# Kernel tuning notes

Measured on AMD Instinct MI355X. Metric: run time of the kernel, lower is better.

Reference implementation:

```python
import math
import jax
import jax.numpy as jnp
import numpy as np

B, L, C = 16, 512, 1024
N_HEAD = 8
HEAD = C // N_HEAD


def setup_inputs() -> dict:
    key = jax.random.key(0)
    k1, k2, k3, k4, k5, k6 = jax.random.split(key, 6)
    x = jax.random.normal(k1, (B, L, C), dtype=jnp.float32)
    # binary adjacency (0/1) as float, as in graph data
    adj = jax.random.randint(k2, (B, L, L), 0, 2).astype(jnp.float32)
    W_qkv = jax.random.normal(k3, (C, 3 * C), dtype=jnp.float32) * (1.0 / math.sqrt(C))
    b_qkv = jax.random.normal(k4, (3 * C,), dtype=jnp.float32) * 0.02
    W_d = jax.random.normal(k5, (1, C), dtype=jnp.float32)
    b_d = jax.random.normal(k6, (C,), dtype=jnp.float32) * 0.02
    return {"x": x, "adj": adj, "W_qkv": W_qkv, "b_qkv": b_qkv, "W_d": W_d, "b_d": b_d}


def reference(x, adj, W_qkv, b_qkv, W_d, b_d):
    # degree gating (self.degree == True)
    degree = adj.sum(-1, keepdims=True)                      # [B,L,1]
    gate = jax.nn.sigmoid(degree @ W_d + b_d)                # [B,L,C]
    x = x * gate
    # fused qkv projection, chunk into qk / res / value
    qkv = x @ W_qkv + b_qkv                                  # [B,L,3C]
    qk, res, value = jnp.split(qkv, 3, axis=-1)
    def heads(t):                                            # [B,L,C] -> [B,H,L,hd]
        return t.reshape(B, L, N_HEAD, HEAD).transpose(0, 2, 1, 3)
    qk, res, value = heads(qk), heads(res), heads(value)
    qk = jax.nn.sigmoid(qk)
    # sigmoid-kernel attention scores
    attn = jnp.einsum("bhld,bhmd->bhlm", qk, qk) / math.sqrt(HEAD)
    # adjacency masking (rel_pos_bias == True)
    attn = jnp.where(adj[:, None, :, :] == 0, 0.0, attn)
    # sum-normalization instead of softmax
    attn = attn / (attn.sum(-1, keepdims=True) + 1e-6)
    out = jnp.einsum("bhlm,bhmd->bhld", attn, value) + res   # residual from qkv chunk
    out = out.transpose(0, 2, 1, 3).reshape(B, L, C)
    return jax.nn.relu(out)
```

## Files before the change

kernel.cpp:

```cpp
#include <hip/hip_runtime.h>
#include <math.h>

#define BDIM 16
#define LDIM 512
#define CDIM 1024
#define NH 8
#define HD 128
#define MROWS (BDIM * LDIM)
#define N3 (3 * CDIM)

typedef unsigned short u16;
typedef unsigned long long u64;
typedef short s8v __attribute__((ext_vector_type(8)));
typedef short s4v __attribute__((ext_vector_type(4)));
typedef float f32x4 __attribute__((ext_vector_type(4)));

__device__ __forceinline__ float sigmoidf_(float z) {
    return 1.0f / (1.0f + __expf(-z));
}
__device__ __forceinline__ u16 f2bf(float f) {
    union { float f; unsigned int u; } v; v.f = f;
    unsigned int u = v.u;
    unsigned int r = (u + 0x7FFFu + ((u >> 16) & 1u)) >> 16;
    return (u16)r;
}
__device__ __forceinline__ float bf2f(u16 b) {
    union { unsigned int u; float f; } v; v.u = ((unsigned int)b) << 16;
    return v.f;
}

__global__ __launch_bounds__(256) void pre_kernel(const float* __restrict__ adj,
                                                  const float* __restrict__ x,
                                                  const float* __restrict__ Wd,
                                                  const float* __restrict__ bd,
                                                  const float* __restrict__ W,
                                                  u16* __restrict__ xg,
                                                  u64* __restrict__ adjbits,
                                                  u16* __restrict__ Wt) {
    __shared__ float wsum[4];
    __shared__ float tile[64][65];
    int t = threadIdx.x;
    if (blockIdx.x < MROWS) {
        int row = blockIdx.x;
        int w = t >> 6, lane = t & 63;
        const float* a = adj + (size_t)row * LDIM;
        float v0 = a[w * 128 + lane];
        float v1 = a[w * 128 + 64 + lane];
        u64 b0 = __ballot(v0 != 0.f);
        u64 b1 = __ballot(v1 != 0.f);
        if (lane == 0) {
            adjbits[(size_t)row * (LDIM / 64) + 2 * w]     = b0;
            adjbits[(size_t)row * (LDIM / 64) + 2 * w + 1] = b1;
        }
        float s = v0 + v1;
        #pragma unroll
        for (int off = 32; off > 0; off >>= 1) s += __shfl_down(s, off);
        if (lane == 0) wsum[w] = s;
        __syncthreads();
        float d = wsum[0] + wsum[1] + wsum[2] + wsum[3];

        float4 xv = ((const float4*)(x + (size_t)row * CDIM))[t];
        float4 wv = ((const float4*)Wd)[t];
        float4 bv = ((const float4*)bd)[t];
        s4v o;
        o.x = (short)f2bf(xv.x * sigmoidf_(d * wv.x + bv.x));
        o.y = (short)f2bf(xv.y * sigmoidf_(d * wv.y + bv.y));
        o.z = (short)f2bf(xv.z * sigmoidf_(d * wv.z + bv.z));
        o.w = (short)f2bf(xv.w * sigmoidf_(d * wv.w + bv.w));
        ((s4v*)(xg + (size_t)row * CDIM))[t] = o;
    } else {
        int bid = blockIdx.x - MROWS;
        int k0 = (bid & 15) * 64, n0 = (bid >> 4) * 64;
        int tx = t & 63, ty = t >> 6;
        #pragma unroll
        for (int yy = ty; yy < 64; yy += 4)
            tile[yy][tx] = W[(size_t)(k0 + yy) * N3 + n0 + tx];
        __syncthreads();
        #pragma unroll
        for (int yy = ty; yy < 64; yy += 4)
            Wt[(size_t)(n0 + yy) * CDIM + k0 + tx] = f2bf(tile[tx][yy]);
    }
}

__global__ __launch_bounds__(256, 3) void gemm_bf16_kernel(const u16* __restrict__ A,
                                                           const u16* __restrict__ Bt,
                                                           const float* __restrict__ bias,
                                                           u16* __restrict__ ksig,
                                                           u16* __restrict__ resb,
                                                           u16* __restrict__ vt) {
    __shared__ __align__(16) u16 As[128 * 64];
    __shared__ __align__(16) u16 Bs[128 * 64];
    int t = threadIdx.x;
    int m0 = blockIdx.y * 128, n0 = blockIdx.x * 128;
    int lane = t & 63, w = t >> 6;
    int i15 = lane & 15, quad = lane >> 4;
    int wm = w >> 1, wn = w & 1;

    f32x4 acc[4][4];
    #pragma unroll
    for (int i = 0; i < 4; ++i)
        #pragma unroll
        for (int j = 0; j < 4; ++j) acc[i][j] = (f32x4)(0.f);

    for (int k0 = 0; k0 < CDIM; k0 += 64) {
        #pragma unroll
        for (int p = 0; p < 4; ++p) {
            int sb = (w * 4 + p) * 64;
            int s = sb + lane;
            int row = s >> 3;
            int seg = (s & 7) ^ (row & 7);
            const u16* ga = A + (size_t)(m0 + row) * CDIM + k0 + seg * 8;
            const u16* gb = Bt + (size_t)(n0 + row) * CDIM + k0 + seg * 8;
            __builtin_amdgcn_global_load_lds(
                (const __attribute__((address_space(1))) unsigned int*)ga,
                (__attribute__((address_space(3))) unsigned int*)&As[sb * 8], 16, 0, 0);
            __builtin_amdgcn_global_load_lds(
                (const __attribute__((address_space(1))) unsigned int*)gb,
                (__attribute__((address_space(3))) unsigned int*)&Bs[sb * 8], 16, 0, 0);
        }
        __syncthreads();
        #pragma unroll
        for (int kc = 0; kc < 2; ++kc) {
            s8v aF[4], bF[4];
            #pragma unroll
            for (int mt = 0; mt < 4; ++mt) {
                int row = wm * 64 + mt * 16 + i15;
                int slot = row * 8 + ((kc * 4 + quad) ^ (i15 & 7));
                aF[mt] = *(const s8v*)&As[slot * 8];
            }
            #pragma unroll
            for (int nt = 0; nt < 4; ++nt) {
                int row = wn * 64 + nt * 16 + i15;
                int slot = row * 8 + ((kc * 4 + quad) ^ (i15 & 7));
                bF[nt] = *(const s8v*)&Bs[slot * 8];
            }
            #pragma unroll
            for (int mt = 0; mt < 4; ++mt)
                #pragma unroll
                for (int nt = 0; nt < 4; ++nt)
                    acc[mt][nt] = __builtin_amdgcn_mfma_f32_16x16x32_bf16(aF[mt], bF[nt], acc[mt][nt], 0, 0, 0);
        }
        __syncthreads();
    }

    int chunk = n0 >> 10;
    #pragma unroll
    for (int nt = 0; nt < 4; ++nt) {
        int ncol = n0 + wn * 64 + nt * 16 + i15;
        float bv = bias[ncol];
        #pragma unroll
        for (int mt = 0; mt < 4; ++mt) {
            int mbase = m0 + wm * 64 + mt * 16 + quad * 4;
            if (chunk == 0) {
                int h = (ncol >> 7) & 7, d = ncol & 127;
                #pragma unroll
                for (int r = 0; r < 4; ++r) {
                    int mrow = mbase + r;
                    int bb = mrow >> 9, l = mrow & 511;
                    ksig[(((size_t)bb * NH + h) * LDIM + l) * HD + d] = f2bf(sigmoidf_(acc[mt][nt][r] + bv));
                }
            } else if (chunk == 1) {
                #pragma unroll
                for (int r = 0; r < 4; ++r) {
                    int mrow = mbase + r;
                    resb[(size_t)mrow * CDIM + (ncol - CDIM)] = f2bf(acc[mt][nt][r] + bv);
                }
            } else {
                int h = (ncol >> 7) & 7, d = ncol & 127;
                int bb = mbase >> 9, l = mbase & 511;
                s4v pk;
                pk.x = (short)f2bf(acc[mt][nt][0] + bv);
                pk.y = (short)f2bf(acc[mt][nt][1] + bv);
                pk.z = (short)f2bf(acc[mt][nt][2] + bv);
                pk.w = (short)f2bf(acc[mt][nt][3] + bv);
                *(s4v*)&vt[(((size_t)bb * NH + h) * HD + d) * LDIM + l] = pk;
            }
        }
    }
}

#define MT 32
#define NITER (LDIM / MT)
__global__ __launch_bounds__(256) void attn_kernel(const u16* __restrict__ ksig,
                                                   const u16* __restrict__ vt,
                                                   const u16* __restrict__ resb,
                                                   const u64* __restrict__ adjbits,
                                                   float* __restrict__ out) {
    __shared__ __align__(16) u16 lds_ks[2][MT * 128];
    __shared__ __align__(16) u16 lds_vt[2][128 * MT];
    __shared__ __align__(16) u16 lds_ps[4][16][40];

    int t = threadIdx.x;
    int lane = t & 63, w = t >> 6;
    int i15 = lane & 15, quad = lane >> 4;
    int bid = blockIdx.x;
    int l0 = (bid >> 7) * 64;
    int b  = (bid >> 3) & 15;
    int h  = bid & 7;

    const u16* ksig_bh = ksig + ((size_t)b * NH + h) * LDIM * HD;
    const u16* vt_bh   = vt + ((size_t)b * NH + h) * HD * LDIM;
    const unsigned int* abits32 = (const unsigned int*)adjbits;
    size_t arow0 = ((size_t)b * LDIM + l0 + w * 16 + quad * 4) * (LDIM / 32);

    s8v aQ[4];
    {
        const u16* qrow = ksig_bh + (size_t)(l0 + w * 16 + i15) * HD + quad * 8;
        #pragma unroll
        for (int kc = 0; kc < 4; ++kc) aQ[kc] = *(const s8v*)(qrow + kc * 32);
    }

    f32x4 accO[8];
    #pragma unroll
    for (int i = 0; i < 8; ++i) accO[i] = (f32x4)(0.f);
    float prs[4] = {0.f, 0.f, 0.f, 0.f};

    const float scale = 0.08838834764831845f;

    auto stage = [&](int m0s, int buf) {
        #pragma unroll
        for (int p = 0; p < 2; ++p) {
            int sb = (w * 2 + p) * 64;
            int s = sb + lane;
            int row = s >> 4;
            int seg = (s & 15) ^ (row & 15);
            const u16* g = ksig_bh + (size_t)(m0s + row) * HD + seg * 8;
            __builtin_amdgcn_global_load_lds(
                (const __attribute__((address_space(1))) unsigned int*)g,
                (__attribute__((address_space(3))) unsigned int*)&lds_ks[buf][sb * 8], 16, 0, 0);
        }
        #pragma unroll
        for (int p = 0; p < 2; ++p) {
            int sb = (w * 2 + p) * 64;
            int s = sb + lane;
            int row = s >> 2;
            int seg = (s & 3) ^ ((row >> 1) & 3);
            const u16* g = vt_bh + (size_t)row * LDIM + m0s + seg * 8;
            __builtin_amdgcn_global_load_lds(
                (const __attribute__((address_space(1))) unsigned int*)g,
                (__attribute__((address_space(3))) unsigned int*)&lds_vt[buf][sb * 8], 16, 0, 0);
        }
    };

    stage(0, 0);
    __syncthreads();

    for (int i = 0; i < NITER; ++i) {
        int cur = i & 1;
        int m0 = i * MT;
        if (i + 1 < NITER) stage(m0 + MT, cur ^ 1);

        unsigned int mw[4];
        #pragma unroll
        for (int r = 0; r < 4; ++r)
            mw[r] = abits32[arow0 + (size_t)r * (LDIM / 32) + i];

        f32x4 S[2];
        #pragma unroll
        for (int nt = 0; nt < 2; ++nt) {
            S[nt] = (f32x4)(0.f);
            int row = nt * 16 + i15;
            #pragma unroll
            for (int kc = 0; kc < 4; ++kc) {
                int slot = row * 16 + ((kc * 4 + quad) ^ (row & 15));
                s8v bK = *(const s8v*)&lds_ks[cur][slot * 8];
                S[nt] = __builtin_amdgcn_mfma_f32_16x16x32_bf16(aQ[kc], bK, S[nt], 0, 0, 0);
            }
        }

        #pragma unroll
        for (int nt = 0; nt < 2; ++nt) {
            int sh = nt * 16 + i15;
            #pragma unroll
            for (int r = 0; r < 4; ++r) {
                float p = ((mw[r] >> sh) & 1u) ? S[nt][r] * scale : 0.f;
                prs[r] += p;
                lds_ps[w][quad * 4 + r][nt * 16 + i15] = f2bf(p);
            }
        }

        {
            s8v aP = *(const s8v*)&lds_ps[w][i15][quad * 8];
            #pragma unroll
            for (int ntd = 0; ntd < 8; ++ntd) {
                int row = ntd * 16 + i15;
                int slot = row * 4 + (quad ^ ((row >> 1) & 3));
                s8v bV = *(const s8v*)&lds_vt[cur][slot * 8];
                accO[ntd] = __builtin_amdgcn_mfma_f32_16x16x32_bf16(aP, bV, accO[ntd], 0, 0, 0);
            }
        }
        if (i + 1 < NITER) __syncthreads();
    }

    float inv[4];
    #pragma unroll
    for (int r = 0; r < 4; ++r) {
        float s = prs[r];
        s += __shfl_xor(s, 1);
        s += __shfl_xor(s, 2);
        s += __shfl_xor(s, 4);
        s += __shfl_xor(s, 8);
        inv[r] = 1.0f / (s + 1e-6f);
    }
    #pragma unroll
    for (int ntd = 0; ntd < 8; ++ntd) {
        int dcol = h * HD + ntd * 16 + i15;
        #pragma unroll
        for (int r = 0; r < 4; ++r) {
            size_t idx = ((size_t)b * LDIM + l0 + w * 16 + quad * 4 + r) * CDIM + dcol;
            float v = accO[ntd][r] * inv[r] + bf2f(resb[idx]);
            out[idx] = fmaxf(v, 0.f);
        }
    }
}

extern "C" void kernel_launch(void* const* d_in, const int* in_sizes, int n_in,
                              void* d_out, int out_size, void* d_ws, size_t ws_size,
                              hipStream_t stream) {
    (void)in_sizes; (void)n_in; (void)out_size; (void)ws_size;
    const float* x     = (const float*)d_in[0];
    const float* adj   = (const float*)d_in[1];
    const float* W_qkv = (const float*)d_in[2];
    const float* b_qkv = (const float*)d_in[3];
    const float* W_d   = (const float*)d_in[4];
    const float* b_d   = (const float*)d_in[5];
    float* out = (float*)d_out;

    char* ws = (char*)d_ws;
    size_t off = 0;
    u64* adjb   = (u64*)(ws + off);   off += (size_t)MROWS * 8 * 8;
    u16*   xg   = (u16*)(ws + off);   off += (size_t)MROWS * CDIM * 2;
    u16*   Wt   = (u16*)(ws + off);   off += (size_t)N3 * CDIM * 2;
    u16*   ksig = (u16*)(ws + off);   off += (size_t)MROWS * CDIM * 2;
    u16*   resb = (u16*)(ws + off);   off += (size_t)MROWS * CDIM * 2;
    u16*   vt   = (u16*)(ws + off);   off += (size_t)MROWS * CDIM * 2;

    pre_kernel<<<MROWS + (CDIM / 64) * (N3 / 64), 256, 0, stream>>>(adj, x, W_d, b_d, W_qkv, xg, adjb, Wt);
    gemm_bf16_kernel<<<dim3(N3 / 128, MROWS / 128), 256, 0, stream>>>(xg, Wt, b_qkv, ksig, resb, vt);
    attn_kernel<<<LDIM / 64 * NH * BDIM, 256, 0, stream>>>(ksig, vt, resb, adjb, out);
}
```

Before: 212.2 us.

## Use 32x32x16 MFMA in QKV GEMM and stage adjacency bits in LDS

The QKV projection GEMM switches from 16x16x32 to 32x32x16 bf16 MFMA tiles, with each wave holding 2x2 accumulators of 16 floats instead of 4x4 of 4. The epilogue is rewritten to match the new output-register layout. This cuts the number of fragment loads and MFMA issues per k-step. Separately, the attention kernel preloads its block's adjacency bitmask rows into LDS once, replacing per-iteration global loads, at the cost of extra shared memory.

New measurement: 214.5 us. Within noise of the previous version (+1.1%).

```diff
diff --git a/kernel.cpp b/kernel.cpp
--- a/kernel.cpp
+++ b/kernel.cpp
@@ -11,9 +11,11 @@
 
 typedef unsigned short u16;
 typedef unsigned long long u64;
+typedef unsigned int u32;
 typedef short s8v __attribute__((ext_vector_type(8)));
 typedef short s4v __attribute__((ext_vector_type(4)));
 typedef float f32x4 __attribute__((ext_vector_type(4)));
+typedef float f32x16 __attribute__((ext_vector_type(16)));
 
 __device__ __forceinline__ float sigmoidf_(float z) {
     return 1.0f / (1.0f + __expf(-z));
@@ -93,14 +95,14 @@
     int t = threadIdx.x;
     int m0 = blockIdx.y * 128, n0 = blockIdx.x * 128;
     int lane = t & 63, w = t >> 6;
-    int i15 = lane & 15, quad = lane >> 4;
+    int i31 = lane & 31, h5 = lane >> 5;
     int wm = w >> 1, wn = w & 1;
 
-    f32x4 acc[4][4];
-    #pragma unroll
-    for (int i = 0; i < 4; ++i)
-        #pragma unroll
-        for (int j = 0; j < 4; ++j) acc[i][j] = (f32x4)(0.f);
+    f32x16 acc[2][2];
+    #pragma unroll
+    for (int i = 0; i < 2; ++i)
+        #pragma unroll
+        for (int j = 0; j < 2; ++j) acc[i][j] = (f32x16)(0.f);
 
     for (int k0 = 0; k0 < CDIM; k0 += 64) {
         #pragma unroll
@@ -120,60 +122,72 @@
         }
         __syncthreads();
         #pragma unroll
-        for (int kc = 0; kc < 2; ++kc) {
-            s8v aF[4], bF[4];
-            #pragma unroll
-            for (int mt = 0; mt < 4; ++mt) {
-                int row = wm * 64 + mt * 16 + i15;
-                int slot = row * 8 + ((kc * 4 + quad) ^ (i15 & 7));
+        for (int kc = 0; kc < 4; ++kc) {
+            s8v aF[2], bF[2];
+            int seg = kc * 2 + h5;
+            #pragma unroll
+            for (int mt = 0; mt < 2; ++mt) {
+                int row = wm * 64 + mt * 32 + i31;
+                int slot = row * 8 + (seg ^ (row & 7));
                 aF[mt] = *(const s8v*)&As[slot * 8];
             }
             #pragma unroll
-            for (int nt = 0; nt < 4; ++nt) {
-                int row = wn * 64 + nt * 16 + i15;
-                int slot = row * 8 + ((kc * 4 + quad) ^ (i15 & 7));
+            for (int nt = 0; nt < 2; ++nt) {
+                int row = wn * 64 + nt * 32 + i31;
+                int slot = row * 8 + (seg ^ (row & 7));
                 bF[nt] = *(const s8v*)&Bs[slot * 8];
             }
             #pragma unroll
-            for (int mt = 0; mt < 4; ++mt)
+            for (int mt = 0; mt < 2; ++mt)
                 #pragma unroll
-                for (int nt = 0; nt < 4; ++nt)
-                    acc[mt][nt] = __builtin_amdgcn_mfma_f32_16x16x32_bf16(aF[mt], bF[nt], acc[mt][nt], 0, 0, 0);
+                for (int nt = 0; nt < 2; ++nt)
+                    acc[mt][nt] = __builtin_amdgcn_mfma_f32_32x32x16_bf16(aF[mt], bF[nt], acc[mt][nt], 0, 0, 0);
         }
         __syncthreads();
     }
 
     int chunk = n0 >> 10;
     #pragma unroll
-    for (int nt = 0; nt < 4; ++nt) {
-        int ncol = n0 + wn * 64 + nt * 16 + i15;
+    for (int nt = 0; nt < 2; ++nt) {
+        int ncol = n0 + wn * 64 + nt * 32 + i31;
         float bv = bias[ncol];
         #pragma unroll
-        for (int mt = 0; mt < 4; ++mt) {
-            int mbase = m0 + wm * 64 + mt * 16 + quad * 4;
+        for (int mt = 0; mt < 2; ++mt) {
+            int mq = m0 + wm * 64 + mt * 32 + 4 * h5;
             if (chunk == 0) {
                 int h = (ncol >> 7) & 7, d = ncol & 127;
                 #pragma unroll
-                for (int r = 0; r < 4; ++r) {
-                    int mrow = mbase + r;
-                    int bb = mrow >> 9, l = mrow & 511;
-                    ksig[(((size_t)bb * NH + h) * LDIM + l) * HD + d] = f2bf(sigmoidf_(acc[mt][nt][r] + bv));
+                for (int g = 0; g < 4; ++g) {
+                    #pragma unroll
+                    for (int r = 0; r < 4; ++r) {
+                        int mrow = mq + 8 * g + r;
+                        int bb = mrow >> 9, l = mrow & 511;
+                        ksig[(((size_t)bb * NH + h) * LDIM + l) * HD + d] =
+                            f2bf(sigmoidf_(acc[mt][nt][4 * g + r] + bv));
+                    }
                 }
             } else if (chunk == 1) {
                 #pragma unroll
-                for (int r = 0; r < 4; ++r) {
-                    int mrow = mbase + r;
-                    resb[(size_t)mrow * CDIM + (ncol - CDIM)] = f2bf(acc[mt][nt][r] + bv);
+                for (int g = 0; g < 4; ++g) {
+                    #pragma unroll
+                    for (int r = 0; r < 4; ++r) {
+                        int mrow = mq + 8 * g + r;
+                        resb[(size_t)mrow * CDIM + (ncol - CDIM)] = f2bf(acc[mt][nt][4 * g + r] + bv);
+                    }
                 }
             } else {
                 int h = (ncol >> 7) & 7, d = ncol & 127;
-                int bb = mbase >> 9, l = mbase & 511;
-                s4v pk;
-                pk.x = (short)f2bf(acc[mt][nt][0] + bv);
-                pk.y = (short)f2bf(acc[mt][nt][1] + bv);
-                pk.z = (short)f2bf(acc[mt][nt][2] + bv);
-                pk.w = (short)f2bf(acc[mt][nt][3] + bv);
-                *(s4v*)&vt[(((size_t)bb * NH + h) * HD + d) * LDIM + l] = pk;
+                #pragma unroll
+                for (int g = 0; g < 4; ++g) {
+                    int mbase = mq + 8 * g;
+                    int bb = mbase >> 9, l = mbase & 511;
+                    s4v pk;
+                    pk.x = (short)f2bf(acc[mt][nt][4 * g + 0] + bv);
+                    pk.y = (short)f2bf(acc[mt][nt][4 * g + 1] + bv);
+                    pk.z = (short)f2bf(acc[mt][nt][4 * g + 2] + bv);
+                    pk.w = (short)f2bf(acc[mt][nt][4 * g + 3] + bv);
+                    *(s4v*)&vt[(((size_t)bb * NH + h) * HD + d) * LDIM + l] = pk;
+                }
             }
         }
     }
@@ -189,6 +203,7 @@
     __shared__ __align__(16) u16 lds_ks[2][MT * 128];
     __shared__ __align__(16) u16 lds_vt[2][128 * MT];
     __shared__ __align__(16) u16 lds_ps[4][16][40];
+    __shared__ u32 lds_adj[64][20];
 
     int t = threadIdx.x;
     int lane = t & 63, w = t >> 6;
@@ -200,8 +215,7 @@
 
     const u16* ksig_bh = ksig + ((size_t)b * NH + h) * LDIM * HD;
     const u16* vt_bh   = vt + ((size_t)b * NH + h) * HD * LDIM;
-    const unsigned int* abits32 = (const unsigned int*)adjbits;
-    size_t arow0 = ((size_t)b * LDIM + l0 + w * 16 + quad * 4) * (LDIM / 32);
+    const u32* abits32 = (const u32*)adjbits;
 
     s8v aQ[4];
     {
@@ -243,17 +257,25 @@
     };
 
     stage(0, 0);
+    {
+        int row = t >> 2, w0 = (t & 3) * 4;
+        const u32* g = abits32 + ((size_t)(b * LDIM + l0 + row) * 16) + w0;
+        uint4 v = *(const uint4*)g;
+        lds_adj[row][w0 + 0] = v.x;
+        lds_adj[row][w0 + 1] = v.y;
+        lds_adj[row][w0 + 2] = v.z;
+        lds_adj[row][w0 + 3] = v.w;
+    }
     __syncthreads();
 
     for (int i = 0; i < NITER; ++i) {
         int cur = i & 1;
-        int m0 = i * MT;
-        if (i + 1 < NITER) stage(m0 + MT, cur ^ 1);
+        if (i + 1 < NITER) stage((i + 1) * MT, cur ^ 1);
 
         unsigned int mw[4];
         #pragma unroll
         for (int r = 0; r < 4; ++r)
-            mw[r] = abits32[arow0 + (size_t)r * (LDIM / 32) + i];
+            mw[r] = lds_adj[w * 16 + quad * 4 + r][i];
 
         f32x4 S[2];
         #pragma unroll
```
